# Performance work log

Hardware: AMD Instinct MI355X
Metric: run time of the kernel (lower is better)

## Reference

```python
import jax, jax.numpy as jnp
import numpy as np

jax.config.update("jax_enable_x64", True)

BATCH = 64
NUM_TRAJ = 128
MAXT = 1.0
DELTAT = 2.0 ** -8
N_STEPS = int(round(MAXT / DELTAT)) - 1  # tvec = arange(0, maxt, dt): 256 points -> 255 Euler steps

_sx = np.array([[0, 1], [1, 0]], dtype=np.complex128)
_sy = np.array([[0, -1j], [1j, 0]], dtype=np.complex128)
_sz = np.array([[1, 0], [0, -1]], dtype=np.complex128)
_I2 = np.eye(2, dtype=np.complex128)

# Two-qubit Rabi weak-measurement operators (d=10 Hermitian state, m=2 noise channels)
HX = jnp.asarray(0.5 * (np.kron(_sx, _I2) + np.kron(_I2, _sx)))  # Rabi drive
HZ = jnp.asarray(0.5 * (np.kron(_sz, _I2) + np.kron(_I2, _sz)))  # detuning
C1 = jnp.asarray(np.kron(_sz, _I2))  # weak measurement channel, qubit 0
C2 = jnp.asarray(np.kron(_I2, _sz))  # weak measurement channel, qubit 1


def _meas_ops():
    # 42 probabilities: 9 joint Pauli-basis pairs x 4 outcomes (36) + single-qubit '+' outcomes (6)
    paulis = [_sx, _sy, _sz]
    ops = []
    for A in paulis:
        for B in paulis:
            for sa in (1, -1):
                for sb in (1, -1):
                    ops.append(np.kron((_I2 + sa * A) / 2, (_I2 + sb * B) / 2))
    for A in paulis:
        ops.append(np.kron((_I2 + A) / 2, _I2))
    for B in paulis:
        ops.append(np.kron(_I2, (_I2 + B) / 2))
    return jnp.asarray(np.stack(ops))  # [42, 4, 4]

MEAS = _meas_ops()


def _forward(inputs, params, wvec, rho0):
    inputs = inputs.astype(jnp.float64)  # [B, 1]
    batch = inputs.shape[0]

    # Build per-trajectory params: column input_param=0 comes from inputs, rest are constants
    cols = [inputs + 1e-8 if ii == 0 else params[ii].astype(jnp.float64) * jnp.ones_like(inputs)
            for ii in range(params.shape[0])]
    traj_p = jnp.concatenate(cols, axis=1)            # [B, 4]
    traj_p = jnp.tile(traj_p, (NUM_TRAJ, 1))          # [N, 4], N = NUM_TRAJ*B
    N = NUM_TRAJ * batch

    rho = jnp.tile(rho0[None].astype(jnp.complex128), (N, 1, 1))  # [N, 4, 4]

    Omega = traj_p[:, 0].astype(jnp.complex128)[:, None, None]
    eps = traj_p[:, 1].astype(jnp.complex128)[:, None, None]
    Gamma = traj_p[:, 2][:, None, None]               # real
    eta = traj_p[:, 3][:, None, None]                 # real, measurement efficiency
    H = Omega * HX + eps * HZ                         # [N, 4, 4]
    sqge = jnp.sqrt(jnp.maximum(Gamma * eta, 0.0))

    def hmeas(r, c):
        # H[c] rho = c rho + rho c - tr(c rho + rho c) rho  (c Hermitian)
        anti = c @ r + r @ c
        tr = jnp.trace(anti, axis1=-2, axis2=-1)[:, None, None]
        return anti - tr * r

    def step(r, dw):                                  # dw: [N, 2] real, ~sqrt(dt) Gaussian
        comm = H @ r - r @ H
        diss = (C1 @ r @ C1 - r) + (C2 @ r @ C2 - r)  # c^2 = I for sigma_z channels
        drift = -1j * comm + Gamma * diss
        noise = sqge * (hmeas(r, C1) * dw[:, 0, None, None]
                        + hmeas(r, C2) * dw[:, 1, None, None])
        return r + drift * DELTAT + noise, None

    dws = jnp.swapaxes(wvec.astype(jnp.float64), 0, 1)  # [T-1, N, 2]
    rho_T, _ = jax.lax.scan(step, rho, dws)

    # Monte-Carlo average over num_traj (matches reduce_mean over axis 0 of [num_traj, B, ...])
    rho_mean = jnp.mean(rho_T.reshape(NUM_TRAJ, batch, 4, 4), axis=0)  # [B, 4, 4]

    probs = jnp.real(jnp.einsum('kij,bji->bk', MEAS, rho_mean))        # tr(M rho), [B, 42]
    probs = jnp.clip(probs, 0.0, 1.0)
    out = jnp.concatenate([probs, inputs], axis=1)                     # [B, 43]
    return out, rho_mean


def setup_inputs() -> dict:
    key = jax.random.key(0)
    k1, k2 = jax.random.split(key)
    inputs = jax.random.uniform(k1, (BATCH, 1), dtype=jnp.float64)
    params = jnp.array([1.0, 0.1, 0.5, 0.8], dtype=jnp.float64)  # [Omega, eps, Gamma, eta]
    wvec = jax.random.normal(k2, (NUM_TRAJ * BATCH, N_STEPS, 2), dtype=jnp.float64) * np.sqrt(DELTAT)
    rho0 = jnp.zeros((4, 4), dtype=jnp.complex128).at[0, 0].set(1.0)  # |00><00|
    return {"inputs": inputs, "params": params, "wvec": wvec, "rho0": rho0}


def reference(inputs, params, wvec, rho0):
    return _forward(inputs, params, wvec, rho0)
```

## Files before the change

### kernel.cpp

```cpp
#include <hip/hip_runtime.h>
#include <math.h>

#define BATCH 64
#define NUM_TRAJ 128
#define NTOT (BATCH*NUM_TRAJ)
#define NSTEPS 255

static constexpr float DT = 0.00390625f;

template<int C>
__device__ __forceinline__ float qp(float x) {
    union { float f; int i; } u;
    u.f = x;
    u.i = __builtin_amdgcn_update_dpp(0, u.i, C, 0xF, 0xF, true);
    return u.f;
}
#define DPP_HALF_MIRROR 0x141

__device__ __forceinline__ float qsum2(float x) { return qp<65>(x) + qp<190>(x); }

__global__ __launch_bounds__(64, 1) void traj_kernel(
    const float* __restrict__ inputs,
    const float* __restrict__ params,
    const float* __restrict__ wvec,
    const float* __restrict__ rho0,
    int rho0_cplx,
    float* __restrict__ ws)
{
    const int tid = blockIdx.x * 64 + threadIdx.x;
    const int g  = tid >> 3;
    const int l8 = tid & 7;
    const int p  = l8 & 3;
    const int c  = l8 >> 2;
    const int r  = c ? (3 - p) : p;
    const int b  = g & (BATCH - 1);

    const float Omega = inputs[b] + 1e-8f;
    const float a     = 0.5f * Omega;
    const float eps   = params[1];
    const float Gamma = params[2];
    const float eta   = params[3];
    const float sqge  = sqrtf(fmaxf(Gamma * eta, 0.0f));
    const float gdt   = Gamma * DT;

    const float s1   = (r < 2) ? 1.0f : -1.0f;
    const float s2   = (r & 1) ? -1.0f : 1.0f;
    const float hr   = (r == 0) ? eps : ((r == 3) ? -eps : 0.0f);
    const int  colA  = c ? 1 : 0;
    const int  colB  = c ? 2 : 3;
    const float s2A  = c ? -1.0f : 1.0f;
    const float coefA = hr - (c ? 0.0f : eps);
    const float coefB = hr + (c ? 0.0f : eps);
    const float dmA  = gdt * ( (s1 + s2 * s2A) - 2.0f);
    const float dmB  = gdt * (-(s1 + s2 * s2A) - 2.0f);
    const float S1   = s1 * sqge;
    const float S2   = s2 * sqge;
    const float SQ   = sqge;
    const float PC2  = (c ? -1.0f : 1.0f) * sqge;
    const float f1   = (r == colA) ? 1.0f : 0.0f;
    const float f2   = (r == colB) ? 1.0f : 0.0f;

    float qa_re, qa_im, qb_re, qb_im;
    {
        const int idxA = r * 4 + colA, idxB = r * 4 + colB;
        if (rho0_cplx) {
            qa_re = rho0[2 * idxA]; qa_im = rho0[2 * idxA + 1];
            qb_re = rho0[2 * idxB]; qb_im = rho0[2 * idxB + 1];
        } else {
            qa_re = rho0[idxA]; qa_im = 0.0f;
            qb_re = rho0[idxB]; qb_im = 0.0f;
        }
    }

    const float2* wp2 = reinterpret_cast<const float2*>(wvec) + (size_t)g * NSTEPS;

    float urc, pownc;

    auto calc_next = [&](float dwA, float dwB) {
        const float pown = fmaf(S1, dwA, S2 * dwB);
        const float tw = pown + pown;
        const float tm = tw * fmaf(f1, qa_re, f2 * qb_re);
        float z = tm;
        z += qp<177>(z);
        z += qp<78>(z);
        z += qp<DPP_HALF_MIRROR>(z);
        urc = z; pownc = pown;
    };

    auto step = [&](float dwA, float dwB) {
        const float u_re = qa_re + qb_re, u_im = qa_im + qb_im;
        const float up_re = qp<DPP_HALF_MIRROR>(u_re);
        const float up_im = qp<DPP_HALF_MIRROR>(u_im);

        const float SA_re = qsum2(qa_re), SA_im = qsum2(qa_im);
        const float SB_re = qsum2(qb_re), SB_im = qsum2(qb_im);

        const float au_re = a * up_re, au_im = a * up_im;
        const float cA_re = fmaf(coefA, qa_re, fmaf(a, SA_re, -au_re));
        const float cA_im = fmaf(coefA, qa_im, fmaf(a, SA_im, -au_im));
        const float cB_re = fmaf(coefB, qb_re, fmaf(a, SB_re, -au_re));
        const float cB_im = fmaf(coefB, qb_im, fmaf(a, SB_im, -au_im));

        const float pc   = fmaf(SQ, dwA, PC2 * dwB);
        const float base = pownc - urc;
        const float WA = (base + dmA) + pc;
        const float WB = (base + dmB) - pc;

        float n_re, n_im;
        n_re = fmaf(DT, cA_im, qa_re);  n_re = fmaf(WA, qa_re, n_re);
        n_im = fmaf(-DT, cA_re, qa_im); n_im = fmaf(WA, qa_im, n_im);
        qa_re = n_re; qa_im = n_im;
        n_re = fmaf(DT, cB_im, qb_re);  n_re = fmaf(WB, qb_re, n_re);
        n_im = fmaf(-DT, cB_re, qb_im); n_im = fmaf(WB, qb_im, n_im);
        qb_re = n_re; qb_im = n_im;
    };

    float2 cw[8], nw[8];
#pragma unroll
    for (int s = 0; s < 8; ++s) cw[s] = wp2[s];
    calc_next(cw[0].x, cw[0].y);
#pragma unroll 1
    for (int T = 0; T < 31; ++T) {
        if (T < 30) {
#pragma unroll
            for (int s = 0; s < 8; ++s) nw[s] = wp2[8 * (T + 1) + s];
        } else {
#pragma unroll
            for (int s = 0; s < 7; ++s) nw[s] = wp2[248 + s];
            nw[7] = make_float2(0.f, 0.f);
        }
#pragma unroll
        for (int s = 0; s < 8; ++s) {
            step(cw[s].x, cw[s].y);
            if (s < 7) calc_next(cw[s + 1].x, cw[s + 1].y);
            else       calc_next(nw[0].x, nw[0].y);
        }
#pragma unroll
        for (int s = 0; s < 8; ++s) cw[s] = nw[s];
    }
#pragma unroll
    for (int s = 0; s < 7; ++s) {
        step(cw[s].x, cw[s].y);
        if (s < 6) calc_next(cw[s + 1].x, cw[s + 1].y);
    }

    float4* o = reinterpret_cast<float4*>(ws + (size_t)g * 32);
    o[c * 4 + r] = make_float4(qa_re, qa_im, qb_re, qb_im);
}

__device__ inline void fill_proj(int p, float s, float pr[2][2], float pim[2][2])
{
    pr[0][0] = 0.5f; pr[0][1] = 0.f; pr[1][0] = 0.f; pr[1][1] = 0.5f;
    pim[0][0] = 0.f; pim[0][1] = 0.f; pim[1][0] = 0.f; pim[1][1] = 0.f;
    const float h = 0.5f * s;
    if (p == 0)      { pr[0][1] += h;  pr[1][0] += h; }
    else if (p == 1) { pim[0][1] -= h; pim[1][0] += h; }
    else             { pr[0][0] += h;  pr[1][1] -= h; }
}

__device__ inline void fill_id(float pr[2][2], float pim[2][2])
{
    pr[0][0] = 1.f; pr[0][1] = 0.f; pr[1][0] = 0.f; pr[1][1] = 1.f;
    pim[0][0] = 0.f; pim[0][1] = 0.f; pim[1][0] = 0.f; pim[1][1] = 0.f;
}

__global__ __launch_bounds__(256) void reduce_meas_kernel(
    const float* __restrict__ ws,
    const float* __restrict__ inputs,
    float* __restrict__ out,
    int out_size)
{
    const int b = blockIdx.x;
    const int tid = threadIdx.x;
    __shared__ float part[8][32];
    __shared__ float sr[16], si[16];

    {
        const int e = tid & 31;
        const int h = tid >> 5;
        const int plane = e >> 4;
        const int el = e & 15;
        const int i = el >> 2, j = el & 3;
        const int cc = (j == 1 || j == 2) ? 1 : 0;
        const int slot = (j == 2 || j == 3) ? 1 : 0;
        const int fidx = (cc * 4 + i) * 4 + slot * 2 + plane;
        float s = 0.f;
#pragma unroll 4
        for (int k = h * 16; k < h * 16 + 16; k++)
            s += ws[((size_t)(k * BATCH + b)) * 32 + fidx];
        part[h][e] = s;
    }
    __syncthreads();
    if (tid < 32) {
        float s = 0.f;
#pragma unroll
        for (int h = 0; h < 8; h++) s += part[h][tid];
        s *= (1.0f / NUM_TRAJ);
        if (tid < 16) sr[tid] = s; else si[tid - 16] = s;
    }
    __syncthreads();

    if (tid < 42) {
        float par[2][2], pai[2][2], pbr[2][2], pbi[2][2];
        const int m = tid;
        if (m < 36) {
            const int ia = m / 12, rem = m - ia * 12;
            const int ib = rem / 4, r2 = rem - ib * 4;
            fill_proj(ia, (r2 & 2) ? -1.f : 1.f, par, pai);
            fill_proj(ib, (r2 & 1) ? -1.f : 1.f, pbr, pbi);
        } else if (m < 39) {
            fill_proj(m - 36, 1.f, par, pai);
            fill_id(pbr, pbi);
        } else {
            fill_id(par, pai);
            fill_proj(m - 39, 1.f, pbr, pbi);
        }
        float prob = 0.f;
#pragma unroll
        for (int a1 = 0; a1 < 2; a1++)
#pragma unroll
            for (int b1 = 0; b1 < 2; b1++)
#pragma unroll
                for (int a2 = 0; a2 < 2; a2++)
#pragma unroll
                    for (int b2 = 0; b2 < 2; b2++) {
                        const int i = 2 * a1 + b1, j = 2 * a2 + b2;
                        const float Mr = par[a1][a2] * pbr[b1][b2] - pai[a1][a2] * pbi[b1][b2];
                        const float Mi = par[a1][a2] * pbi[b1][b2] + pai[a1][a2] * pbr[b1][b2];
                        prob += Mr * sr[j * 4 + i] - Mi * si[j * 4 + i];
                    }
        prob = fminf(fmaxf(prob, 0.f), 1.f);
        out[b * 43 + m] = prob;
    } else if (tid == 42) {
        out[b * 43 + 42] = inputs[b];
    }

    if (out_size >= 2752 + 2048) {
        if (tid < 16) {
            out[2752 + b * 32 + 2 * tid]     = sr[tid];
            out[2752 + b * 32 + 2 * tid + 1] = si[tid];
        }
    } else if (out_size >= 2752 + 1024) {
        if (tid < 16) out[2752 + b * 16 + tid] = sr[tid];
    }
}

extern "C" void kernel_launch(void* const* d_in, const int* in_sizes, int n_in,
                              void* d_out, int out_size, void* d_ws, size_t ws_size,
                              hipStream_t stream)
{
    const float* inputs = (const float*)d_in[0];
    const float* params = (const float*)d_in[1];
    const float* wvec   = (const float*)d_in[2];
    const float* rho0   = (const float*)d_in[3];
    const int rho0_cplx = (n_in > 3 && in_sizes[3] >= 32) ? 1 : 0;
    float* ws = (float*)d_ws;

    traj_kernel<<<(NTOT * 8) / 64, 64, 0, stream>>>(inputs, params, wvec, rho0, rho0_cplx, ws);
    reduce_meas_kernel<<<BATCH, 256, 0, stream>>>(ws, inputs, (float*)d_out, out_size);
}
```

Baseline: 32.19 us.

## Process two trajectories per thread to interleave independent recurrences

Each thread now advances two independent trajectories, offset by half the total, with interleaved step and reduction calls, and the grid is halved. This is meant to expose instruction-level parallelism that hides DPP and FMA latency in the serial time-stepping chain. In exchange it doubles per-thread register state and halves the number of waves available for latency hiding across CUs.

```diff
diff --git a/kernel.cpp b/kernel.cpp
--- a/kernel.cpp
+++ b/kernel.cpp
@@ -28,12 +28,14 @@
     float* __restrict__ ws)
 {
     const int tid = blockIdx.x * 64 + threadIdx.x;
-    const int g  = tid >> 3;
+    const int h  = tid >> 3;
     const int l8 = tid & 7;
+    const int g1 = h;
+    const int g2 = h + NTOT / 2;
     const int p  = l8 & 3;
     const int c  = l8 >> 2;
     const int r  = c ? (3 - p) : p;
-    const int b  = g & (BATCH - 1);
+    const int b  = g1 & (BATCH - 1);
 
     const float Omega = inputs[b] + 1e-8f;
     const float a     = 0.5f * Omega;
@@ -60,23 +62,29 @@
     const float f1   = (r == colA) ? 1.0f : 0.0f;
     const float f2   = (r == colB) ? 1.0f : 0.0f;
 
-    float qa_re, qa_im, qb_re, qb_im;
+    float a1r, a1i, b1r, b1i;
+    float a2r, a2i, b2r, b2i;
     {
         const int idxA = r * 4 + colA, idxB = r * 4 + colB;
+        float xar, xai, xbr, xbi;
         if (rho0_cplx) {
-            qa_re = rho0[2 * idxA]; qa_im = rho0[2 * idxA + 1];
-            qb_re = rho0[2 * idxB]; qb_im = rho0[2 * idxB + 1];
+            xar = rho0[2 * idxA]; xai = rho0[2 * idxA + 1];
+            xbr = rho0[2 * idxB]; xbi = rho0[2 * idxB + 1];
         } else {
-            qa_re = rho0[idxA]; qa_im = 0.0f;
-            qb_re = rho0[idxB]; qb_im = 0.0f;
-        }
-    }
-
-    const float2* wp2 = reinterpret_cast<const float2*>(wvec) + (size_t)g * NSTEPS;
-
-    float urc, pownc;
-
-    auto calc_next = [&](float dwA, float dwB) {
+            xar = rho0[idxA]; xai = 0.0f;
+            xbr = rho0[idxB]; xbi = 0.0f;
+        }
+        a1r = xar; a1i = xai; b1r = xbr; b1i = xbi;
+        a2r = xar; a2i = xai; b2r = xbr; b2i = xbi;
+    }
+
+    const float2* w1 = reinterpret_cast<const float2*>(wvec) + (size_t)g1 * NSTEPS;
+    const float2* w2 = reinterpret_cast<const float2*>(wvec) + (size_t)g2 * NSTEPS;
+
+    float ur1, pn1, ur2, pn2;
+
+    auto calc_next = [&](float qa_re, float qb_re, float dwA, float dwB,
+                         float& urc, float& pownc) {
         const float pown = fmaf(S1, dwA, S2 * dwB);
         const float tw = pown + pown;
         const float tm = tw * fmaf(f1, qa_re, f2 * qb_re);
@@ -87,7 +95,8 @@
         urc = z; pownc = pown;
     };
 
-    auto step = [&](float dwA, float dwB) {
+    auto step = [&](float& qa_re, float& qa_im, float& qb_re, float& qb_im,
+                    float urc, float pownc, float dwA, float dwB) {
         const float u_re = qa_re + qb_re, u_im = qa_im + qb_im;
         const float up_re = qp<DPP_HALF_MIRROR>(u_re);
         const float up_im = qp<DPP_HALF_MIRROR>(u_im);
@@ -115,37 +124,50 @@
         qb_re = n_re; qb_im = n_im;
     };
 
-    float2 cw[8], nw[8];
-#pragma unroll
-    for (int s = 0; s < 8; ++s) cw[s] = wp2[s];
-    calc_next(cw[0].x, cw[0].y);
+    float2 c1[8], n1[8], c2[8], n2[8];
+#pragma unroll
+    for (int s = 0; s < 8; ++s) { c1[s] = w1[s]; c2[s] = w2[s]; }
+    calc_next(a1r, b1r, c1[0].x, c1[0].y, ur1, pn1);
+    calc_next(a2r, b2r, c2[0].x, c2[0].y, ur2, pn2);
 #pragma unroll 1
     for (int T = 0; T < 31; ++T) {
         if (T < 30) {
 #pragma unroll
-            for (int s = 0; s < 8; ++s) nw[s] = wp2[8 * (T + 1) + s];
+            for (int s = 0; s < 8; ++s) { n1[s] = w1[8 * (T + 1) + s]; n2[s] = w2[8 * (T + 1) + s]; }
         } else {
 #pragma unroll
-            for (int s = 0; s < 7; ++s) nw[s] = wp2[248 + s];
-            nw[7] = make_float2(0.f, 0.f);
+            for (int s = 0; s < 7; ++s) { n1[s] = w1[248 + s]; n2[s] = w2[248 + s]; }
+            n1[7] = make_float2(0.f, 0.f); n2[7] = make_float2(0.f, 0.f);
         }
 #pragma unroll
         for (int s = 0; s < 8; ++s) {
-            step(cw[s].x, cw[s].y);
-            if (s < 7) calc_next(cw[s + 1].x, cw[s + 1].y);
-            else       calc_next(nw[0].x, nw[0].y);
-        }
-#pragma unroll
-        for (int s = 0; s < 8; ++s) cw[s] = nw[s];
+            step(a1r, a1i, b1r, b1i, ur1, pn1, c1[s].x, c1[s].y);
+            step(a2r, a2i, b2r, b2i, ur2, pn2, c2[s].x, c2[s].y);
+            if (s < 7) {
+                calc_next(a1r, b1r, c1[s + 1].x, c1[s + 1].y, ur1, pn1);
+                calc_next(a2r, b2r, c2[s + 1].x, c2[s + 1].y, ur2, pn2);
+            } else {
+                calc_next(a1r, b1r, n1[0].x, n1[0].y, ur1, pn1);
+                calc_next(a2r, b2r, n2[0].x, n2[0].y, ur2, pn2);
+            }
+        }
+#pragma unroll
+        for (int s = 0; s < 8; ++s) { c1[s] = n1[s]; c2[s] = n2[s]; }
     }
 #pragma unroll
     for (int s = 0; s < 7; ++s) {
-        step(cw[s].x, cw[s].y);
-        if (s < 6) calc_next(cw[s + 1].x, cw[s + 1].y);
-    }
-
-    float4* o = reinterpret_cast<float4*>(ws + (size_t)g * 32);
-    o[c * 4 + r] = make_float4(qa_re, qa_im, qb_re, qb_im);
+        step(a1r, a1i, b1r, b1i, ur1, pn1, c1[s].x, c1[s].y);
+        step(a2r, a2i, b2r, b2i, ur2, pn2, c2[s].x, c2[s].y);
+        if (s < 6) {
+            calc_next(a1r, b1r, c1[s + 1].x, c1[s + 1].y, ur1, pn1);
+            calc_next(a2r, b2r, c2[s + 1].x, c2[s + 1].y, ur2, pn2);
+        }
+    }
+
+    float4* o1 = reinterpret_cast<float4*>(ws + (size_t)g1 * 32);
+    o1[c * 4 + r] = make_float4(a1r, a1i, b1r, b1i);
+    float4* o2 = reinterpret_cast<float4*>(ws + (size_t)g2 * 32);
+    o2[c * 4 + r] = make_float4(a2r, a2i, b2r, b2i);
 }
 
 __device__ inline void fill_proj(int p, float s, float pr[2][2], float pim[2][2])
@@ -256,6 +278,6 @@
     const int rho0_cplx = (n_in > 3 && in_sizes[3] >= 32) ? 1 : 0;
     float* ws = (float*)d_ws;
 
-    traj_kernel<<<(NTOT * 8) / 64, 64, 0, stream>>>(inputs, params, wvec, rho0, rho0_cplx, ws);
+    traj_kernel<<<(NTOT * 8 / 2) / 64, 64, 0, stream>>>(inputs, params, wvec, rho0, rho0_cplx, ws);
     reduce_meas_kernel<<<BATCH, 256, 0, stream>>>(ws, inputs, (float*)d_out, out_size);
 }
```

Result: slower. 54.02 us (+67.8%).
